# Performance work log

Measured on AMD Instinct MI355X. Metric: run time of the kernel, lower is better.

The kernel has to match this reference:

```python
import jax, jax.numpy as jnp
import numpy as np

# Static config (matches init_kwargs)
DIM = 1024
INTER = 512
E = 8          # n_routed_experts
TOP_K = 2      # n_activated_experts
ROUTE_SCALE = 1.0


def setup_inputs() -> dict:
    key = jax.random.key(0)
    ks = jax.random.split(key, 8)
    s_d = 1.0 / np.sqrt(DIM)
    s_f = 1.0 / np.sqrt(INTER)
    x = jax.random.normal(ks[0], (2, 2048, DIM), dtype=jnp.float32)
    gate_w = jax.random.uniform(ks[1], (E, DIM), jnp.float32, -s_d, s_d)
    # routed expert weights, stacked: gate/up are [E, F, D], down is [E, D, F]
    wg = jax.random.uniform(ks[2], (E, INTER, DIM), jnp.float32, -s_d, s_d)
    wu = jax.random.uniform(ks[3], (E, INTER, DIM), jnp.float32, -s_d, s_d)
    wd = jax.random.uniform(ks[4], (E, DIM, INTER), jnp.float32, -s_f, s_f)
    # shared expert (n_shared_experts = 1)
    sg = jax.random.uniform(ks[5], (INTER, DIM), jnp.float32, -s_d, s_d)
    su = jax.random.uniform(ks[6], (INTER, DIM), jnp.float32, -s_d, s_d)
    sd = jax.random.uniform(ks[7], (DIM, INTER), jnp.float32, -s_f, s_f)
    return {"x": x, "gate_w": gate_w, "wg": wg, "wu": wu, "wd": wd,
            "sg": sg, "su": su, "sd": sd}


def reference(x, gate_w, wg, wu, wd, sg, su, sd):
    B, S, D = x.shape
    xf = x.reshape(-1, D)                       # [N, D]
    N = xf.shape[0]

    # ---- Gate (eval mode: no expert_bias, softmax scoring, 1 group) ----
    scores = jax.nn.softmax(xf @ gate_w.T, axis=-1)          # [N, E]
    _, idx = jax.lax.top_k(scores, TOP_K)                    # [N, K]
    weights = jnp.take_along_axis(scores, idx, axis=-1) * ROUTE_SCALE  # [N, K]

    # Combine weights as dense [N, E] (scatter-add of top-k weights) --
    # equivalent to the sort/dispatch + weighted scatter_add combine.
    cw = jnp.zeros((N, E), dtype=xf.dtype)
    cw = cw.at[jnp.arange(N)[:, None], idx].add(weights)     # [N, E]

    # ---- Routed experts: SwiGLU per expert ----
    g = jnp.einsum('nd,efd->nef', xf, wg)                    # [N, E, F]
    u = jnp.einsum('nd,efd->nef', xf, wu)                    # [N, E, F]
    h = jax.nn.silu(g) * u                                   # [N, E, F]
    y = jnp.einsum('nef,edf->ned', h, wd)                    # [N, E, D]
    routed = jnp.einsum('ned,ne->nd', y, cw)                 # [N, D]

    # ---- Shared expert (always active) ----
    shared = (jax.nn.silu(xf @ sg.T) * (xf @ su.T)) @ sd.T   # [N, D]

    return (routed + shared).reshape(B, S, D)
```

## Files before the change

kernel.cpp:

```cpp
#include <hip/hip_runtime.h>
#include <hip/hip_bf16.h>

constexpr int NTOK = 4096;
constexpr int DIMD = 1024;
constexpr int FINT = 512;
constexpr int NEXP = 8;

typedef __attribute__((ext_vector_type(8))) short bf16x8;
typedef __attribute__((ext_vector_type(4))) float f32x4;
typedef __attribute__((ext_vector_type(8))) unsigned short u16x8;

__device__ __forceinline__ f32x4 mfma16(bf16x8 a, bf16x8 b, f32x4 c) {
  return __builtin_amdgcn_mfma_f32_16x16x32_bf16(a, b, c, 0, 0, 0);
}

__device__ __forceinline__ void gload16(const void* g, void* l) {
  __builtin_amdgcn_global_load_lds(
      (const __attribute__((address_space(1))) void*)g,
      (__attribute__((address_space(3))) void*)l, 16, 0, 0);
}

__device__ __forceinline__ unsigned short f2bf(float f) {
  unsigned u = __float_as_uint(f);
  u += 0x7fffu + ((u >> 16) & 1u);
  return (unsigned short)(u >> 16);
}

__global__ __launch_bounds__(256) void cast_all(
    const float* __restrict__ x,  const float* __restrict__ wg,
    const float* __restrict__ wu, const float* __restrict__ wd,
    const float* __restrict__ sg, const float* __restrict__ su,
    const float* __restrict__ sd, const float* __restrict__ gw,
    unsigned short* __restrict__ xb,  unsigned short* __restrict__ w1b,
    unsigned short* __restrict__ wdb, unsigned short* __restrict__ s1b,
    unsigned short* __restrict__ sdb,
    int* __restrict__ eid, float2* __restrict__ w12) {
  const int seg = blockIdx.y;

  if (seg == 7) {
    if (blockIdx.x >= NTOK / 4) return;
    const int wid = threadIdx.x >> 6;
    const int lane = threadIdx.x & 63;
    const int n = blockIdx.x * 4 + wid;

    const float4* xr = (const float4*)(x + (size_t)n * DIMD);
    float4 xv[4];
#pragma unroll
    for (int j = 0; j < 4; ++j) xv[j] = xr[lane + 64 * j];

    double acc[NEXP];
#pragma unroll
    for (int e = 0; e < NEXP; ++e) {
      const float4* g = (const float4*)(gw + (size_t)e * DIMD);
      double a = 0.0;
#pragma unroll
      for (int j = 0; j < 4; ++j) {
        float4 gv = g[lane + 64 * j];
        a += (double)xv[j].x * (double)gv.x + (double)xv[j].y * (double)gv.y
           + (double)xv[j].z * (double)gv.z + (double)xv[j].w * (double)gv.w;
      }
      acc[e] = a;
    }
#pragma unroll
    for (int e = 0; e < NEXP; ++e) {
#pragma unroll
      for (int off = 32; off > 0; off >>= 1) acc[e] += __shfl_xor(acc[e], off);
    }

    if (lane == 0) {
      float logit[NEXP];
#pragma unroll
      for (int e = 0; e < NEXP; ++e) logit[e] = (float)acc[e];
      int i1 = 0; float v1 = logit[0];
#pragma unroll
      for (int e = 1; e < NEXP; ++e) if (logit[e] > v1) { v1 = logit[e]; i1 = e; }
      int i2 = -1; float v2 = -1e30f;
#pragma unroll
      for (int e = 0; e < NEXP; ++e) if (e != i1 && logit[e] > v2) { v2 = logit[e]; i2 = e; }
      float s = 0.f;
#pragma unroll
      for (int e = 0; e < NEXP; ++e) s += expf(logit[e] - v1);
      float w1 = 1.f / s;
      float w2 = expf(v2 - v1) / s;
      eid[n] = i1 | (i2 << 4);
      w12[n] = make_float2(w1, w2);
    }
    return;
  }

  const int i = blockIdx.x * 256 + threadIdx.x;
  const float* src; unsigned short* dst;
  size_t si = (size_t)i * 8, di;
  int n8;
  if (seg == 0) {
    n8 = NTOK * DIMD / 8; if (i >= n8) return;
    src = x; dst = xb; di = si;
  } else if (seg == 1 || seg == 2) {
    n8 = NEXP * FINT * DIMD / 8; if (i >= n8) return;
    int e = (int)(si >> 19), f = (int)((si >> 10) & 511), d = (int)(si & 1023);
    int r = ((f >> 4) << 5) + (seg == 2 ? 16 : 0) + (f & 15);
    src = (seg == 1) ? wg : wu; dst = w1b;
    di = (((size_t)e << 10) + r) * 1024 + d;
  } else if (seg == 3) {
    n8 = NEXP * DIMD * FINT / 8; if (i >= n8) return;
    src = wd; dst = wdb; di = si;
  } else if (seg == 4 || seg == 5) {
    n8 = FINT * DIMD / 8; if (i >= n8) return;
    int f = (int)((si >> 10) & 511), d = (int)(si & 1023);
    int r = ((f >> 4) << 5) + (seg == 5 ? 16 : 0) + (f & 15);
    src = (seg == 4) ? sg : su; dst = s1b;
    di = (size_t)r * 1024 + d;
  } else {
    n8 = DIMD * FINT / 8; if (i >= n8) return;
    src = sd; dst = sdb; di = si;
  }
  const float4* s4 = (const float4*)(src + si);
  float4 a = s4[0], b = s4[1];
  u16x8 o;
  o[0] = f2bf(a.x); o[1] = f2bf(a.y); o[2] = f2bf(a.z); o[3] = f2bf(a.w);
  o[4] = f2bf(b.x); o[5] = f2bf(b.y); o[6] = f2bf(b.z); o[7] = f2bf(b.w);
  *(u16x8*)(dst + di) = o;
}

__global__ __launch_bounds__(1024) void dispatch_scan(const int* __restrict__ eid,
                                                      const float2* __restrict__ w12,
                                                      int* __restrict__ cnt,
                                                      int* __restrict__ rowTok,
                                                      float* __restrict__ rowW,
                                                      int2* __restrict__ gslot) {
  const int th = threadIdx.x;
  const int lane = th & 63;
  const int wv = th >> 6;

  int e0[4], e1[4];
  float2 wp[4];
  unsigned long long c0 = 0, c1 = 0;
#pragma unroll
  for (int j = 0; j < 4; ++j) {
    int n = th * 4 + j;
    int p = eid[n];
    wp[j] = w12[n];
    int a = p & 15, b = (p >> 4) & 15;
    e0[j] = a; e1[j] = b;
    unsigned long long ia = 1ull << (16 * (a & 3));
    if (a < 4) c0 += ia; else c1 += ia;
    unsigned long long ib = 1ull << (16 * (b & 3));
    if (b < 4) c0 += ib; else c1 += ib;
  }

  unsigned long long s0 = c0, s1 = c1;
#pragma unroll
  for (int off = 1; off < 64; off <<= 1) {
    unsigned long long u0 = __shfl_up(s0, off);
    unsigned long long u1 = __shfl_up(s1, off);
    if (lane >= off) { s0 += u0; s1 += u1; }
  }

  __shared__ unsigned long long wt0[16], wt1[16];
  __shared__ int ebaseS[NEXP];
  if (lane == 63) { wt0[wv] = s0; wt1[wv] = s1; }
  __syncthreads();

  unsigned long long b0 = 0, b1 = 0;
  for (int w2 = 0; w2 < 16; ++w2)
    if (w2 < wv) { b0 += wt0[w2]; b1 += wt1[w2]; }

  if (th == 0) {
    unsigned long long t0 = 0, t1 = 0;
    for (int w2 = 0; w2 < 16; ++w2) { t0 += wt0[w2]; t1 += wt1[w2]; }
    int tot[NEXP];
#pragma unroll
    for (int e = 0; e < 4; ++e) {
      tot[e]     = (int)((t0 >> (16 * e)) & 0xffff);
      tot[e + 4] = (int)((t1 >> (16 * e)) & 0xffff);
    }
    int run = 0;
#pragma unroll
    for (int e = 0; e < NEXP; ++e) {
      cnt[e] = tot[e];
      cnt[8 + e] = run;
      ebaseS[e] = run;
      run += tot[e];
    }
  }

  unsigned long long x0 = b0 + s0 - c0;
  unsigned long long x1 = b1 + s1 - c1;

  __shared__ unsigned short posL[1024][8];
#pragma unroll
  for (int e = 0; e < 4; ++e) {
    posL[th][e]     = (unsigned short)((x0 >> (16 * e)) & 0xffff);
    posL[th][e + 4] = (unsigned short)((x1 >> (16 * e)) & 0xffff);
  }
  __syncthreads();

#pragma unroll
  for (int j = 0; j < 4; ++j) {
    int n = th * 4 + j;
    int a = e0[j];
    int pa = posL[th][a]; posL[th][a] = (unsigned short)(pa + 1);
    rowTok[a * NTOK + pa] = n; rowW[a * NTOK + pa] = wp[j].x;
    int b = e1[j];
    int pb = posL[th][b]; posL[th][b] = (unsigned short)(pb + 1);
    rowTok[b * NTOK + pb] = n; rowW[b * NTOK + pb] = wp[j].y;
    gslot[n] = make_int2(ebaseS[a] + pa, ebaseS[b] + pb);
  }
}


__global__ __launch_bounds__(512, 1) void gemm1_fused(
    const unsigned short* __restrict__ xb,
    const unsigned short* __restrict__ w1b,
    const unsigned short* __restrict__ s1b,
    unsigned short* __restrict__ hb,
    unsigned short* __restrict__ hs,
    const int* __restrict__ cnt,
    const int* __restrict__ rowTok,
    const unsigned short* __restrict__ zpg) {
  extern __shared__ unsigned char L[];
  const int e = blockIdx.x >> 2, ty = blockIdx.x & 3;
  const int tx = blockIdx.y;
  const bool RT = (e < NEXP);
  const int Te = RT ? cnt[e] : NTOK;
  const int m0 = tx * 256;
  if (m0 >= Te) return;
  const int n0 = ty * 256;

  const int t = threadIdx.x;
  const int w = t >> 6, lane = t & 63;
  const int wr = w >> 2, wc = w & 3;
  const int fr = lane & 15, hi = lane >> 4;
  const int koffl = ((hi ^ ((fr >> 1) & 3)) << 4);

  const unsigned short* w1e = RT ? w1b + (size_t)e * DIMD * DIMD : s1b;

  const unsigned short* apD[2];
  const unsigned short* bpD[2];
  int aoff[2], boff[2];
#pragma unroll
  for (int j = 0; j < 2; ++j) {
    int c = w * 128 + j * 64 + lane;
    int rowL = c >> 2;
    int seff = (c & 3) ^ ((c >> 3) & 3);
    int grow = m0 + rowL;
    const unsigned short* p;
    if (RT) p = (grow < Te) ? xb + (size_t)rowTok[e * NTOK + grow] * DIMD : zpg;
    else    p = xb + (size_t)grow * DIMD;
    apD[j] = p + seff * 8;
    bpD[j] = w1e + (size_t)(n0 + rowL) * DIMD + seff * 8;
    aoff[j] = c * 16;
    boff[j] = 65536 + c * 16;
  }

  f32x4 acc[8][4];
  f32x4 zero = {0.f, 0.f, 0.f, 0.f};
#pragma unroll
  for (int m = 0; m < 8; ++m)
#pragma unroll
    for (int n = 0; n < 4; ++n) acc[m][n] = zero;

  auto STAGE = [&](int buf, int tt, int q) {
    int slab = (buf * 2 + q) * 16384;
#pragma unroll
    for (int j = 0; j < 2; ++j) {
      gload16(apD[j] + tt * 64 + q * 32, L + slab + aoff[j]);
      gload16(bpD[j] + tt * 64 + q * 32, L + slab + boff[j]);
    }
  };
  auto TILE = [&](int buf) {
    bf16x8 Af[2][8], Bf[2][4];
#pragma unroll
    for (int q = 0; q < 2; ++q) {
      int slab = (buf * 2 + q) * 16384;
      const unsigned char* LA = L + slab;
      const unsigned char* LB = L + 65536 + slab;
#pragma unroll
      for (int m = 0; m < 8; ++m)
        Af[q][m] = *(const bf16x8*)(LA + (wr * 128 + m * 16 + fr) * 64 + koffl);
#pragma unroll
      for (int n = 0; n < 4; ++n)
        Bf[q][n] = *(const bf16x8*)(LB + (wc * 64 + n * 16 + fr) * 64 + koffl);
    }
    __builtin_amdgcn_s_setprio(1);
#pragma unroll
    for (int q = 0; q < 2; ++q)
#pragma unroll
      for (int n = 0; n < 4; ++n)
#pragma unroll
        for (int m = 0; m < 8; ++m)
          acc[m][n] = mfma16(Af[q][m], Bf[q][n], acc[m][n]);
    __builtin_amdgcn_s_setprio(0);
  };

  STAGE(0, 0, 0);
  STAGE(0, 0, 1);

  constexpr int NT = DIMD / 64;
  for (int tt = 0; tt < NT; ++tt) {
    int buf = tt & 1;
    if (tt + 1 < NT) { STAGE(buf ^ 1, tt + 1, 0); STAGE(buf ^ 1, tt + 1, 1); }
    if (tt + 1 < NT) asm volatile("s_waitcnt vmcnt(8)" ::: "memory");
    else             asm volatile("s_waitcnt vmcnt(0)" ::: "memory");
    __builtin_amdgcn_sched_barrier(0);
    __builtin_amdgcn_s_barrier();
    __builtin_amdgcn_sched_barrier(0);
    TILE(buf);
    __builtin_amdgcn_sched_barrier(0);
    __builtin_amdgcn_s_barrier();
  }

  unsigned short* hbase = RT ? hb + (size_t)cnt[8 + e] * FINT : hs;
  const int fbase = ty * 128 + wc * 32 + fr;
#pragma unroll
  for (int m = 0; m < 8; ++m) {
#pragma unroll
    for (int r = 0; r < 4; ++r) {
      int row = m0 + wr * 128 + m * 16 + hi * 4 + r;
      if (row < Te) {
        float g0 = acc[m][0][r], u0 = acc[m][1][r];
        float g1 = acc[m][2][r], u1 = acc[m][3][r];
        hbase[(size_t)row * FINT + fbase]      = f2bf(g0 / (1.f + expf(-g0)) * u0);
        hbase[(size_t)row * FINT + fbase + 16] = f2bf(g1 / (1.f + expf(-g1)) * u1);
      }
    }
  }
}

__global__ __launch_bounds__(512, 1) void gemm2_fused(
    const unsigned short* __restrict__ hb,
    const unsigned short* __restrict__ hs,
    const unsigned short* __restrict__ wdb,
    const unsigned short* __restrict__ sdb,
    float* __restrict__ ybuf,
    float* __restrict__ out,
    const int* __restrict__ cnt,
    const float* __restrict__ rowW,
    const unsigned short* __restrict__ zpg) {
  extern __shared__ unsigned char L[];
  const int e = blockIdx.x >> 2, ty = blockIdx.x & 3;
  const int tx = blockIdx.y;
  const bool RT = (e < NEXP);
  const int Te = RT ? cnt[e] : NTOK;
  const int m0 = tx * 256;
  if (m0 >= Te) return;
  const int n0 = ty * 256;

  const int t = threadIdx.x;
  const int w = t >> 6, lane = t & 63;
  const int wr = w >> 2, wc = w & 3;
  const int fr = lane & 15, hi = lane >> 4;
  const int koffl = ((hi ^ ((fr >> 1) & 3)) << 4);

  const int gbase = RT ? cnt[8 + e] : 0;
  const unsigned short* he  = RT ? hb + (size_t)gbase * FINT : hs;
  const unsigned short* wde = RT ? wdb + (size_t)e * DIMD * FINT : sdb;

  const unsigned short* apD[2];
  const unsigned short* bpD[2];
  int aoff[2], boff[2];
#pragma unroll
  for (int j = 0; j < 2; ++j) {
    int c = w * 128 + j * 64 + lane;
    int rowL = c >> 2;
    int seff = (c & 3) ^ ((c >> 3) & 3);
    int grow = m0 + rowL;
    apD[j] = ((grow < Te) ? he + (size_t)grow * FINT : zpg) + seff * 8;
    bpD[j] = wde + (size_t)(n0 + rowL) * FINT + seff * 8;
    aoff[j] = c * 16;
    boff[j] = 65536 + c * 16;
  }

  f32x4 acc[8][4];
  f32x4 zero = {0.f, 0.f, 0.f, 0.f};
#pragma unroll
  for (int m = 0; m < 8; ++m)
#pragma unroll
    for (int n = 0; n < 4; ++n) acc[m][n] = zero;

  auto STAGE = [&](int buf, int tt, int q) {
    int slab = (buf * 2 + q) * 16384;
#pragma unroll
    for (int j = 0; j < 2; ++j) {
      gload16(apD[j] + tt * 64 + q * 32, L + slab + aoff[j]);
      gload16(bpD[j] + tt * 64 + q * 32, L + slab + boff[j]);
    }
  };
  auto TILE = [&](int buf) {
    bf16x8 Af[2][8], Bf[2][4];
#pragma unroll
    for (int q = 0; q < 2; ++q) {
      int slab = (buf * 2 + q) * 16384;
      const unsigned char* LA = L + slab;
      const unsigned char* LB = L + 65536 + slab;
#pragma unroll
      for (int m = 0; m < 8; ++m)
        Af[q][m] = *(const bf16x8*)(LA + (wr * 128 + m * 16 + fr) * 64 + koffl);
#pragma unroll
      for (int n = 0; n < 4; ++n)
        Bf[q][n] = *(const bf16x8*)(LB + (wc * 64 + n * 16 + fr) * 64 + koffl);
    }
    __builtin_amdgcn_s_setprio(1);
#pragma unroll
    for (int q = 0; q < 2; ++q)
#pragma unroll
      for (int n = 0; n < 4; ++n)
#pragma unroll
        for (int m = 0; m < 8; ++m)
          acc[m][n] = mfma16(Af[q][m], Bf[q][n], acc[m][n]);
    __builtin_amdgcn_s_setprio(0);
  };

  STAGE(0, 0, 0);
  STAGE(0, 0, 1);

  constexpr int NT = FINT / 64;
  for (int tt = 0; tt < NT; ++tt) {
    int buf = tt & 1;
    if (tt + 1 < NT) { STAGE(buf ^ 1, tt + 1, 0); STAGE(buf ^ 1, tt + 1, 1); }
    if (tt + 1 < NT) asm volatile("s_waitcnt vmcnt(8)" ::: "memory");
    else             asm volatile("s_waitcnt vmcnt(0)" ::: "memory");
    __builtin_amdgcn_sched_barrier(0);
    __builtin_amdgcn_s_barrier();
    __builtin_amdgcn_sched_barrier(0);
    TILE(buf);
    __builtin_amdgcn_sched_barrier(0);
    __builtin_amdgcn_s_barrier();
  }

  const int colb = n0 + wc * 64;
#pragma unroll
  for (int m = 0; m < 8; ++m) {
#pragma unroll
    for (int r = 0; r < 4; ++r) {
      int row = m0 + wr * 128 + m * 16 + hi * 4 + r;
      if (row < Te) {
        if (RT) {
          float wt = rowW[e * NTOK + row];
          float* yr = ybuf + (size_t)(gbase + row) * DIMD;
#pragma unroll
          for (int n = 0; n < 4; ++n)
            yr[colb + n * 16 + fr] = wt * acc[m][n][r];
        } else {
          float* orow = out + (size_t)row * DIMD;
#pragma unroll
          for (int n = 0; n < 4; ++n)
            orow[colb + n * 16 + fr] = acc[m][n][r];
        }
      }
    }
  }
}

__global__ __launch_bounds__(256) void combine(const float* __restrict__ ybuf,
                                               const int2* __restrict__ gslot,
                                               float* __restrict__ out) {
  const int n = blockIdx.x;
  const int t = threadIdx.x;
  int2 gs = gslot[n];
  const float4* y1 = (const float4*)(ybuf + (size_t)gs.x * DIMD);
  const float4* y2 = (const float4*)(ybuf + (size_t)gs.y * DIMD);
  float4* o = (float4*)(out + (size_t)n * DIMD);
  float4 a = o[t], b = y1[t], c = y2[t];
  a.x += b.x + c.x; a.y += b.y + c.y; a.z += b.z + c.z; a.w += b.w + c.w;
  o[t] = a;
}

extern "C" void kernel_launch(void* const* d_in, const int* in_sizes, int n_in,
                              void* d_out, int out_size, void* d_ws, size_t ws_size,
                              hipStream_t stream) {
  const float* x  = (const float*)d_in[0];
  const float* gw = (const float*)d_in[1];
  const float* wg = (const float*)d_in[2];
  const float* wu = (const float*)d_in[3];
  const float* wd = (const float*)d_in[4];
  const float* sg = (const float*)d_in[5];
  const float* su = (const float*)d_in[6];
  const float* sd = (const float*)d_in[7];
  float* out = (float*)d_out;

  char* ws = (char*)d_ws;
  size_t off = 0;
  auto alloc = [&](size_t bytes) -> char* {
    char* p = ws + off;
    off += (bytes + 255) & ~(size_t)255;
    return p;
  };
  unsigned short* xb  = (unsigned short*)alloc((size_t)NTOK * DIMD * 2);
  unsigned short* w1b = (unsigned short*)alloc((size_t)NEXP * DIMD * DIMD * 2);
  unsigned short* wdb = (unsigned short*)alloc((size_t)NEXP * DIMD * FINT * 2);
  unsigned short* s1b = (unsigned short*)alloc((size_t)DIMD * DIMD * 2);
  unsigned short* sdb = (unsigned short*)alloc((size_t)DIMD * FINT * 2);
  unsigned short* hb  = (unsigned short*)alloc((size_t)2 * NTOK * FINT * 2);
  unsigned short* hs  = (unsigned short*)alloc((size_t)NTOK * FINT * 2);
  float*         ybuf = (float*)alloc((size_t)2 * NTOK * DIMD * 4);
  int*            cnt = (int*)alloc(256);
  int*         rowTok = (int*)alloc((size_t)NEXP * NTOK * 4);
  float*         rowW = (float*)alloc((size_t)NEXP * NTOK * 4);
  unsigned short* zpg = (unsigned short*)alloc((size_t)DIMD * 2);
  int*            eid = (int*)alloc((size_t)NTOK * 4);
  float2*         w12 = (float2*)alloc((size_t)NTOK * 8);
  int2*         gslot = (int2*)alloc((size_t)NTOK * 8);
  if (off > ws_size) return;

  hipFuncSetAttribute((const void*)gemm1_fused,
                      hipFuncAttributeMaxDynamicSharedMemorySize, 131072);
  hipFuncSetAttribute((const void*)gemm2_fused,
                      hipFuncAttributeMaxDynamicSharedMemorySize, 131072);

  hipMemsetAsync(zpg, 0, (size_t)DIMD * 2, stream);

  cast_all<<<dim3(2048, 8), 256, 0, stream>>>(x, wg, wu, wd, sg, su, sd, gw,
                                              xb, w1b, wdb, s1b, sdb, eid, w12);

  dispatch_scan<<<1, 1024, 0, stream>>>(eid, w12, cnt, rowTok, rowW, gslot);

  gemm1_fused<<<dim3(36, 16), 512, 131072, stream>>>(xb, w1b, s1b, hb, hs,
                                                     cnt, rowTok, zpg);
  gemm2_fused<<<dim3(36, 16), 512, 131072, stream>>>(hb, hs, wdb, sdb, ybuf, out,
                                                     cnt, rowW, zpg);
  combine<<<NTOK, 256, 0, stream>>>(ybuf, gslot, out);
}
```

Before: 125.7 us.

## Interleave half-K LDS staging with MFMA compute in expert GEMM loops

Replaces the per-tile routine, which loaded all A/B fragments and then ran every MFMA, with a finer-grained pipeline shared by both GEMM kernels through one macro. Each k-half gets its own vmcnt wait and barrier, and the next tile's global-to-LDS staging is issued between the two MFMA halves. The trailing per-iteration barrier is dropped. The aim is to overlap global loads with compute and cut fragment register pressure (Af[4] instead of Af[2][8]), at the cost of more barriers per iteration and a tighter scheduling dependency.

```diff
diff --git a/kernel.cpp b/kernel.cpp
--- a/kernel.cpp
+++ b/kernel.cpp
@@ -209,6 +209,79 @@
 }
 
 
+#define GEMM_TILE_LOOP(NT)                                                     \
+  STAGE(0, 0, 0);                                                              \
+  STAGE(0, 0, 1);                                                              \
+  for (int tt = 0; tt < (NT); ++tt) {                                          \
+    const int buf = tt & 1;                                                    \
+    const unsigned char* LA0 = L + (buf * 2 + 0) * 16384;                      \
+    const unsigned char* LB0 = LA0 + 65536;                                    \
+    const unsigned char* LA1 = L + (buf * 2 + 1) * 16384;                      \
+    const unsigned char* LB1 = LA1 + 65536;                                    \
+    bf16x8 Af[4], Bf[4];                                                       \
+                                                            \
+    asm volatile("s_waitcnt vmcnt(4)" ::: "memory");                           \
+    __builtin_amdgcn_sched_barrier(0);                                         \
+    __builtin_amdgcn_s_barrier();                                              \
+    __builtin_amdgcn_sched_barrier(0);                                         \
+    _Pragma("unroll")                                                          \
+    for (int n = 0; n < 4; ++n)                                                \
+      Bf[n] = *(const bf16x8*)(LB0 + (wc * 64 + n * 16 + fr) * 64 + koffl);    \
+    _Pragma("unroll")                                                          \
+    for (int m = 0; m < 4; ++m)                                                \
+      Af[m] = *(const bf16x8*)(LA0 + (wr * 128 + m * 16 + fr) * 64 + koffl);   \
+    __builtin_amdgcn_s_setprio(1);                                             \
+    _Pragma("unroll")                                                          \
+    for (int n = 0; n < 4; ++n)                                                \
+      _Pragma("unroll")                                                        \
+      for (int m = 0; m < 4; ++m)                                              \
+        acc[m][n] = mfma16(Af[m], Bf[n], acc[m][n]);                           \
+    __builtin_amdgcn_s_setprio(0);                                             \
+                                                            \
+    if (tt + 1 < (NT)) STAGE(buf ^ 1, tt + 1, 0);                              \
+    _Pragma("unroll")                                                          \
+    for (int m = 0; m < 4; ++m)                                                \
+      Af[m] = *(const bf16x8*)(LA0 + (wr * 128 + (m + 4) * 16 + fr) * 64 + koffl); \
+    __builtin_amdgcn_s_setprio(1);                                             \
+    _Pragma("unroll")                                                          \
+    for (int n = 0; n < 4; ++n)                                                \
+      _Pragma("unroll")                                                        \
+      for (int m = 0; m < 4; ++m)                                              \
+        acc[m + 4][n] = mfma16(Af[m], Bf[n], acc[m + 4][n]);                   \
+    __builtin_amdgcn_s_setprio(0);                                             \
+                                                            \
+    if (tt + 1 < (NT)) asm volatile("s_waitcnt vmcnt(4)" ::: "memory");        \
+    else               asm volatile("s_waitcnt vmcnt(0)" ::: "memory");        \
+    __builtin_amdgcn_sched_barrier(0);                                         \
+    __builtin_amdgcn_s_barrier();                                              \
+    __builtin_amdgcn_sched_barrier(0);                                         \
+    _Pragma("unroll")                                                          \
+    for (int n = 0; n < 4; ++n)                                                \
+      Bf[n] = *(const bf16x8*)(LB1 + (wc * 64 + n * 16 + fr) * 64 + koffl);    \
+    _Pragma("unroll")                                                          \
+    for (int m = 0; m < 4; ++m)                                                \
+      Af[m] = *(const bf16x8*)(LA1 + (wr * 128 + m * 16 + fr) * 64 + koffl);   \
+    __builtin_amdgcn_s_setprio(1);                                             \
+    _Pragma("unroll")                                                          \
+    for (int n = 0; n < 4; ++n)                                                \
+      _Pragma("unroll")                                                        \
+      for (int m = 0; m < 4; ++m)                                              \
+        acc[m][n] = mfma16(Af[m], Bf[n], acc[m][n]);                           \
+    __builtin_amdgcn_s_setprio(0);                                             \
+                                                            \
+    if (tt + 1 < (NT)) STAGE(buf ^ 1, tt + 1, 1);                              \
+    _Pragma("unroll")                                                          \
+    for (int m = 0; m < 4; ++m)                                                \
+      Af[m] = *(const bf16x8*)(LA1 + (wr * 128 + (m + 4) * 16 + fr) * 64 + koffl); \
+    __builtin_amdgcn_s_setprio(1);                                             \
+    _Pragma("unroll")                                                          \
+    for (int n = 0; n < 4; ++n)                                                \
+      _Pragma("unroll")                                                        \
+      for (int m = 0; m < 4; ++m)                                              \
+        acc[m + 4][n] = mfma16(Af[m], Bf[n], acc[m + 4][n]);                   \
+    __builtin_amdgcn_s_setprio(0);                                             \
+  }
+
 __global__ __launch_bounds__(512, 1) void gemm1_fused(
     const unsigned short* __restrict__ xb,
     const unsigned short* __restrict__ w1b,
@@ -268,47 +341,8 @@
       gload16(bpD[j] + tt * 64 + q * 32, L + slab + boff[j]);
     }
   };
-  auto TILE = [&](int buf) {
-    bf16x8 Af[2][8], Bf[2][4];
-#pragma unroll
-    for (int q = 0; q < 2; ++q) {
-      int slab = (buf * 2 + q) * 16384;
-      const unsigned char* LA = L + slab;
-      const unsigned char* LB = L + 65536 + slab;
-#pragma unroll
-      for (int m = 0; m < 8; ++m)
-        Af[q][m] = *(const bf16x8*)(LA + (wr * 128 + m * 16 + fr) * 64 + koffl);
-#pragma unroll
-      for (int n = 0; n < 4; ++n)
-        Bf[q][n] = *(const bf16x8*)(LB + (wc * 64 + n * 16 + fr) * 64 + koffl);
-    }
-    __builtin_amdgcn_s_setprio(1);
-#pragma unroll
-    for (int q = 0; q < 2; ++q)
-#pragma unroll
-      for (int n = 0; n < 4; ++n)
-#pragma unroll
-        for (int m = 0; m < 8; ++m)
-          acc[m][n] = mfma16(Af[q][m], Bf[q][n], acc[m][n]);
-    __builtin_amdgcn_s_setprio(0);
-  };
-
-  STAGE(0, 0, 0);
-  STAGE(0, 0, 1);
-
-  constexpr int NT = DIMD / 64;
-  for (int tt = 0; tt < NT; ++tt) {
-    int buf = tt & 1;
-    if (tt + 1 < NT) { STAGE(buf ^ 1, tt + 1, 0); STAGE(buf ^ 1, tt + 1, 1); }
-    if (tt + 1 < NT) asm volatile("s_waitcnt vmcnt(8)" ::: "memory");
-    else             asm volatile("s_waitcnt vmcnt(0)" ::: "memory");
-    __builtin_amdgcn_sched_barrier(0);
-    __builtin_amdgcn_s_barrier();
-    __builtin_amdgcn_sched_barrier(0);
-    TILE(buf);
-    __builtin_amdgcn_sched_barrier(0);
-    __builtin_amdgcn_s_barrier();
-  }
+
+  GEMM_TILE_LOOP(DIMD / 64)
 
   unsigned short* hbase = RT ? hb + (size_t)cnt[8 + e] * FINT : hs;
   const int fbase = ty * 128 + wc * 32 + fr;
@@ -386,47 +420,8 @@
       gload16(bpD[j] + tt * 64 + q * 32, L + slab + boff[j]);
     }
   };
-  auto TILE = [&](int buf) {
-    bf16x8 Af[2][8], Bf[2][4];
-#pragma unroll
-    for (int q = 0; q < 2; ++q) {
-      int slab = (buf * 2 + q) * 16384;
-      const unsigned char* LA = L + slab;
-      const unsigned char* LB = L + 65536 + slab;
-#pragma unroll
-      for (int m = 0; m < 8; ++m)
-        Af[q][m] = *(const bf16x8*)(LA + (wr * 128 + m * 16 + fr) * 64 + koffl);
-#pragma unroll
-      for (int n = 0; n < 4; ++n)
-        Bf[q][n] = *(const bf16x8*)(LB + (wc * 64 + n * 16 + fr) * 64 + koffl);
-    }
-    __builtin_amdgcn_s_setprio(1);
-#pragma unroll
-    for (int q = 0; q < 2; ++q)
-#pragma unroll
-      for (int n = 0; n < 4; ++n)
-#pragma unroll
-        for (int m = 0; m < 8; ++m)
-          acc[m][n] = mfma16(Af[q][m], Bf[q][n], acc[m][n]);
-    __builtin_amdgcn_s_setprio(0);
-  };
-
-  STAGE(0, 0, 0);
-  STAGE(0, 0, 1);
-
-  constexpr int NT = FINT / 64;
-  for (int tt = 0; tt < NT; ++tt) {
-    int buf = tt & 1;
-    if (tt + 1 < NT) { STAGE(buf ^ 1, tt + 1, 0); STAGE(buf ^ 1, tt + 1, 1); }
-    if (tt + 1 < NT) asm volatile("s_waitcnt vmcnt(8)" ::: "memory");
-    else             asm volatile("s_waitcnt vmcnt(0)" ::: "memory");
-    __builtin_amdgcn_sched_barrier(0);
-    __builtin_amdgcn_s_barrier();
-    __builtin_amdgcn_sched_barrier(0);
-    TILE(buf);
-    __builtin_amdgcn_sched_barrier(0);
-    __builtin_amdgcn_s_barrier();
-  }
+
+  GEMM_TILE_LOOP(FINT / 64)
 
   const int colb = n0 + wc * 64;
 #pragma unroll
```

New measurement: 111.9 us. -11.0%, faster.
